# Kernel optimization log

Measured on AMD Instinct MI355X. Metric: run time of the kernel, lower is better.

Reference implementation:

```python
import jax, jax.numpy as jnp
import numpy as np

B, SQ, SE, SI, SEI = 16, 512, 512, 256, 768
D, H = 1024, 16
DK = D // H
L1, L2 = 0.5, 0.5
NEG = -1e30  # stand-in for -inf masked_fill


def setup_inputs() -> dict:
    key = jax.random.key(0)
    ks = jax.random.split(key, 32)
    f = lambda i, shp: jax.random.normal(ks[i], shp, dtype=jnp.float32)
    w = lambda i: f(i, (D, D)) * (1.0 / np.sqrt(D))
    b = lambda i: jnp.zeros((D,), jnp.float32)
    inp = {
        'q': f(0, (B, SQ, D)),
        'k_e': f(1, (B, SE, D)), 'v_e': f(2, (B, SE, D)),
        'k_i': f(3, (B, SI, D)), 'v_i': f(4, (B, SI, D)),
        'k_ei': f(5, (B, SEI, D)), 'v_ei': f(6, (B, SEI, D)),
        'mask_e': jax.random.randint(ks[7], (B, SQ, SE), 0, 2) == 1,
        'mask_ei': jax.random.randint(ks[8], (B, SQ, SEI), 0, 2) == 1,
        'e_padding_mask': jax.random.randint(ks[9], (B, SE), 0, 2) == 1,
        'ei_padding_mask': jax.random.randint(ks[10], (B, SEI), 0, 2) == 1,
        'Wq': w(11), 'bq': b(11),
        'Wke': w(12), 'bke': b(12), 'Wve': w(13), 'bve': b(13),
        'Wki': w(14), 'bki': b(14), 'Wvi': w(15), 'bvi': b(15),
        'Wkei': w(16), 'bkei': b(16), 'Wvei': w(17), 'bvei': b(17),
        'Wout': w(18), 'bout': b(18),
    }
    return inp


def _proj(x, W, b):
    # (B, S, D) -> (B, H, S, DK)
    B_, S_, _ = x.shape
    return (x @ W + b).reshape(B_, S_, H, DK).transpose(0, 2, 1, 3)


def _attn(qh, kh, vh, mask, pad_mask):
    # qh: (B,H,Sq,DK), kh/vh: (B,H,Sk,DK)
    s = jnp.einsum('bhqd,bhkd->bhqk', qh, kh) / np.sqrt(DK)
    if mask is not None:
        s = jnp.where(mask[:, None, :, :], NEG, s)
    if pad_mask is not None:
        s = jnp.where(pad_mask[:, None, None, :], NEG, s)
    w = jax.nn.softmax(s, axis=-1)
    # dropout in original is applied to a discarded temp (eval / no-op)
    return jnp.einsum('bhqk,bhkd->bhqd', w, vh), w


def reference(q, k_e, k_i, k_ei, v_e, v_i, v_ei,
              mask_e, mask_ei, e_padding_mask, ei_padding_mask,
              Wq, bq, Wke, bke, Wve, bve, Wki, bki, Wvi, bvi,
              Wkei, bkei, Wvei, bvei, Wout, bout):
    qh = _proj(q, Wq, bq)
    o_e, aw_e = _attn(qh, _proj(k_e, Wke, bke), _proj(v_e, Wve, bve), mask_e, e_padding_mask)
    o_i, aw_i = _attn(qh, _proj(k_i, Wki, bki), _proj(v_i, Wvi, bvi), None, None)
    o_ei, _ = _attn(qh, _proj(k_ei, Wkei, bkei), _proj(v_ei, Wvei, bvei), mask_ei, ei_padding_mask)
    scores = o_e + L1 * o_i + L2 * o_ei  # (B,H,Sq,DK)
    concat = scores.transpose(0, 2, 1, 3).reshape(B, SQ, D)
    output = concat @ Wout + bout
    return output, aw_e, aw_i
```

## Files before the change

### kernel.cpp

```cpp
#include <hip/hip_runtime.h>
#include <stdint.h>

typedef __attribute__((ext_vector_type(8))) short bf16x8;
typedef __attribute__((ext_vector_type(4))) short s16x4;
typedef __attribute__((ext_vector_type(4))) float f32x4;

__device__ __forceinline__ short f2bf(float f){
  unsigned x = __float_as_uint(f);
  unsigned r = (x + 0x7fffu + ((x >> 16) & 1u)) >> 16;
  return (short)r;
}

__device__ __forceinline__ void g2l16(const void* g, void* l){
  __builtin_amdgcn_global_load_lds(
      (const __attribute__((address_space(1))) unsigned int*)(unsigned long long)(uintptr_t)g,
      (__attribute__((address_space(3))) unsigned int*)(unsigned int)(uintptr_t)l,
      16, 0, 0);
}

struct C4 { const float* in[4]; short* out[4]; int n8[4]; };
__global__ __launch_bounds__(256) void cvt4(C4 c){
  const int z = blockIdx.z;
  const int i = blockIdx.x * 256 + threadIdx.x;
  if (i >= c.n8[z]) return;
  const float4* p = (const float4*)c.in[z] + (size_t)i * 2;
  const float4 a = p[0], b = p[1];
  bf16x8 v;
  v[0] = f2bf(a.x); v[1] = f2bf(a.y); v[2] = f2bf(a.z); v[3] = f2bf(a.w);
  v[4] = f2bf(b.x); v[5] = f2bf(b.y); v[6] = f2bf(b.z); v[7] = f2bf(b.w);
  *(bf16x8*)(c.out[z] + (size_t)i * 8) = v;
}

__global__ __launch_bounds__(256)
void make_bits(const int* __restrict__ mask, const int* __restrict__ pad,
               unsigned* __restrict__ bits, int SK){
  const int s = blockIdx.x * 256 + threadIdx.x;
  const size_t row = blockIdx.y;
  const int b = (int)(row >> 9);
  const bool v = (mask[row * SK + s] != 0) || (pad[(size_t)b * SK + s] != 0);
  unsigned long long bal = __ballot(v);
  const int lane = threadIdx.x & 63;
  if ((lane & 31) == 0)
    bits[(row * SK + s) >> 5] = (unsigned)(bal >> (lane & 32));
}

struct W8 { const float* w[8]; };
__global__ __launch_bounds__(256) void pack_w8(W8 ws8, short* __restrict__ out){
  const int m = blockIdx.y;
  const float* __restrict__ W = ws8.w[m];
  short* o = out + (size_t)m * 1048576 + (size_t)blockIdx.x * 4096;
  const int kt = blockIdx.x & 31, nt = blockIdx.x >> 5;
  const int t = threadIdx.x;
  #pragma unroll
  for (int i = 0; i < 16; ++i){
    int flat = i * 256 + t;
    int kl = flat >> 7;
    int nl = flat & 127;
    o[nl * 32 + kl] = f2bf(W[(size_t)(kt * 32 + kl) * 1024 + nt * 128 + nl]);
  }
}

struct GSeg { const short* A; const short* Wp; const float* bias; void* C; int om; int S; int mt; };
struct G4 { GSeg s[4]; };
__global__ __launch_bounds__(256)
void gemm128b(G4 g){
  const GSeg sg = g.s[blockIdx.z];
  if (blockIdx.x >= sg.mt) return;
  __shared__ short sA[2][4096];
  __shared__ short sB[2][4096];
  const int t = threadIdx.x;
  const int m0 = blockIdx.x * 128;
  const int nt = blockIdx.y;
  const int n0 = nt * 128;
  const int w = t >> 6, lane = t & 63, lr = lane & 15, lg = lane >> 4;
  const int wm = (w >> 1) * 64, wn = (w & 1) * 64;

  const int arow  = t >> 2;
  const int acol8 = (t & 3) * 8;
  const short* Ag = sg.A + (size_t)(m0 + arow) * 1024 + acol8;
  const short* Bg = sg.Wp + (size_t)nt * 32 * 4096 + t * 8;

  f32x4 acc[4][4] = {};

  {
    g2l16(Ag, sA[0] + t * 8);
    g2l16(Ag + 64 * 1024, sA[0] + 2048 + t * 8);
    g2l16(Bg, sB[0] + t * 8);
    g2l16(Bg + 2048, sB[0] + 2048 + t * 8);
  }

  int cur = 0;
  for (int kt = 0; kt < 32; ++kt){
    __syncthreads();
    if (kt < 31){
      const int kn = kt + 1;
      g2l16(Ag + kn * 32, sA[cur ^ 1] + t * 8);
      g2l16(Ag + 64 * 1024 + kn * 32, sA[cur ^ 1] + 2048 + t * 8);
      const short* bt = Bg + (size_t)kn * 4096;
      g2l16(bt, sB[cur ^ 1] + t * 8);
      g2l16(bt + 2048, sB[cur ^ 1] + 2048 + t * 8);
    }

    bf16x8 af[4], bfr[4];
    #pragma unroll
    for (int mi = 0; mi < 4; ++mi)
      af[mi] = *(const bf16x8*)&sA[cur][(wm + mi * 16 + lr) * 32 + lg * 8];
    #pragma unroll
    for (int ni = 0; ni < 4; ++ni)
      bfr[ni] = *(const bf16x8*)&sB[cur][(wn + ni * 16 + lr) * 32 + lg * 8];
    #pragma unroll
    for (int mi = 0; mi < 4; ++mi)
      #pragma unroll
      for (int ni = 0; ni < 4; ++ni)
        acc[mi][ni] = __builtin_amdgcn_mfma_f32_16x16x32_bf16(
            af[mi], bfr[ni], acc[mi][ni], 0, 0, 0);
    cur ^= 1;
  }

  #pragma unroll
  for (int ni = 0; ni < 4; ++ni){
    const int n = n0 + wn + ni * 16 + lr;
    const float bv = sg.bias[n];
    #pragma unroll
    for (int mi = 0; mi < 4; ++mi){
      const int mb = m0 + wm + mi * 16 + lg * 4;
      if (sg.om == 0){
        short* C = (short*)sg.C;
        #pragma unroll
        for (int j = 0; j < 4; ++j)
          C[(size_t)(mb + j) * 1024 + n] = f2bf(acc[mi][ni][j] + bv);
      } else if (sg.om == 1){
        short* C = (short*)sg.C;
        const int bb = mb / sg.S, sb = mb % sg.S;
        const int hh = n >> 6, dk = n & 63;
        s16x4 pk;
        #pragma unroll
        for (int j = 0; j < 4; ++j) pk[j] = f2bf(acc[mi][ni][j] + bv);
        *(s16x4*)&C[(((size_t)bb * 16 + hh) * 64 + dk) * sg.S + sb] = pk;
      } else {
        float* C = (float*)sg.C;
        #pragma unroll
        for (int j = 0; j < 4; ++j)
          C[(size_t)(mb + j) * 1024 + n] = acc[mi][ni][j] + bv;
      }
    }
  }
}

template<int SK, bool HAS_BIAS, bool SINGLE>
__device__ __forceinline__ void attn_mod(
    const short* __restrict__ Kp, const short* __restrict__ Vt,
    const unsigned* __restrict__ bits, float* __restrict__ aw,
    const bf16x8 (&qf)[2], f32x4 (&tot)[4], float wgt,
    short* sK, short* sV, short* sPw,
    int b, int h, int qw, int w, int lane, int lr, int lg){
  constexpr int NT  = SK / 128;
  constexpr int SKW = SK / 32;
  static_assert((NT & 1) == 0, "buffer-parity argument needs even NT");

  const int kchunk = (lane & 7) ^ ((lane >> 3) & 7);
  const short* Ksrc = Kp + ((size_t)b * SK + w * 16 + (lane >> 3)) * 1024 + h * 64 + kchunk * 8;
  const short* Vsrc = Vt + ((size_t)(b * 16 + h)) * 64 * SK;
  const int ldoff = w * 1024 + lane * 8;

  const unsigned* bitrow[4];
  if (HAS_BIAS){
    #pragma unroll
    for (int j = 0; j < 4; ++j)
      bitrow[j] = bits + ((size_t)(b * 512 + qw + lg * 4 + j)) * SKW;
  }

  float lrow[4];
  #pragma unroll
  for (int j = 0; j < 4; ++j) lrow[j] = 0.f;
  f32x4 acco[4] = {};

#define SKB(c) (sK + (c) * 8192)
#define SVB(c) (sV + (c) * 8192)
#define STAGE_K(c, s0) do{ \
    g2l16(Ksrc + (size_t)(s0) * 1024, SKB(c) + ldoff); \
    g2l16(Ksrc + (size_t)((s0) + 8) * 1024, SKB(c) + ldoff + 512); }while(0)
#define STAGE_V(c, s0) do{ \
    const int dd0 = w * 8 + (lane >> 4); \
    const int cg0 = (lane & 15) ^ (dd0 & 15); \
    g2l16(Vsrc + (size_t)dd0 * SK + (s0) + cg0 * 8, SVB(c) + ldoff); \
    const int dd1 = dd0 + 4; \
    const int cg1 = (lane & 15) ^ (dd1 & 15); \
    g2l16(Vsrc + (size_t)dd1 * SK + (s0) + cg1 * 8, SVB(c) + ldoff + 512); }while(0)

  if (!SINGLE){
    STAGE_K(0, 0);
    int cur = 0;
    for (int tt = 0; tt < NT; ++tt){
      __syncthreads();
      if (tt + 1 < NT) STAGE_K(cur ^ 1, (tt + 1) * 128);
      const short* kb = SKB(cur);

      f32x4 accs[8];
      #pragma unroll
      for (int si = 0; si < 8; ++si){
        f32x4 a = {};
        #pragma unroll
        for (int dt = 0; dt < 2; ++dt){
          bf16x8 kf = *(const bf16x8*)&kb[(si * 16 + lr) * 64 + ((dt * 4 + lg) ^ (lr & 7)) * 8];
          a = __builtin_amdgcn_mfma_f32_16x16x32_bf16(qf[dt], kf, a, 0, 0, 0);
        }
        accs[si] = a;
      }

      #pragma unroll
      for (int j = 0; j < 4; ++j){
        unsigned wb[4];
        if (HAS_BIAS){
          #pragma unroll
          for (int sp = 0; sp < 4; ++sp) wb[sp] = bitrow[j][tt * 4 + sp];
        }
        float ssum = 0.f;
        #pragma unroll
        for (int si = 0; si < 8; ++si){
          float v = accs[si][j] * 0.125f;
          if (HAS_BIAS && ((wb[si >> 1] >> ((si & 1) * 16 + lr)) & 1u)) v = -1e30f;
          ssum += __expf(v);
        }
        lrow[j] += ssum;
      }
      cur ^= 1;
    }

    #pragma unroll
    for (int j = 0; j < 4; ++j){
      #pragma unroll
      for (int d = 1; d < 16; d <<= 1) lrow[j] += __shfl_xor(lrow[j], d);
    }
    float rinv[4];
    #pragma unroll
    for (int j = 0; j < 4; ++j) rinv[j] = lrow[j] > 0.f ? 1.0f / lrow[j] : 0.f;

    STAGE_K(0, 0);
    STAGE_V(0, 0);
    cur = 0;
    for (int tt = 0; tt < NT; ++tt){
      const int s0 = tt * 128;
      __syncthreads();
      if (tt + 1 < NT){ STAGE_K(cur ^ 1, s0 + 128); STAGE_V(cur ^ 1, s0 + 128); }
      const short* kb = SKB(cur);
      const short* vb = SVB(cur);

      f32x4 accs[8];
      #pragma unroll
      for (int si = 0; si < 8; ++si){
        f32x4 a = {};
        #pragma unroll
        for (int dt = 0; dt < 2; ++dt){
          bf16x8 kf = *(const bf16x8*)&kb[(si * 16 + lr) * 64 + ((dt * 4 + lg) ^ (lr & 7)) * 8];
          a = __builtin_amdgcn_mfma_f32_16x16x32_bf16(qf[dt], kf, a, 0, 0, 0);
        }
        accs[si] = a;
      }

      #pragma unroll
      for (int half = 0; half < 2; ++half){
        #pragma unroll
        for (int j = 0; j < 4; ++j){
          unsigned wb[2];
          if (HAS_BIAS){
            #pragma unroll
            for (int sp = 0; sp < 2; ++sp) wb[sp] = bitrow[j][tt * 4 + half * 2 + sp];
          }
          const int qq = lg * 4 + j;
          float* awrow = aw + (((size_t)(b * 16 + h)) * 512 + qw + qq) * SK + s0 + half * 64 + lr;
          #pragma unroll
          for (int si2 = 0; si2 < 4; ++si2){
            const int si = half * 4 + si2;
            float v = accs[si][j] * 0.125f;
            if (HAS_BIAS && ((wb[si2 >> 1] >> ((si2 & 1) * 16 + lr)) & 1u)) v = -1e30f;
            const float p = __expf(v) * rinv[j];
            __builtin_nontemporal_store(p, &awrow[si2 * 16]);
            sPw[qq * 64 + (((si2 * 2 + (lr >> 3)) ^ (qq & 7)) * 8) + (lr & 7)] = f2bf(p);
          }
        }
        #pragma unroll
        for (int kt2 = 0; kt2 < 2; ++kt2){
          const int kt = half * 2 + kt2;
          bf16x8 pa = *(const bf16x8*)&sPw[lr * 64 + (((kt2 * 4 + lg) ^ (lr & 7)) * 8)];
          #pragma unroll
          for (int ni = 0; ni < 4; ++ni){
            bf16x8 vf = *(const bf16x8*)&vb[(ni * 16 + lr) * 128 + ((kt * 4 + lg) ^ lr) * 8];
            acco[ni] = __builtin_amdgcn_mfma_f32_16x16x32_bf16(pa, vf, acco[ni], 0, 0, 0);
          }
        }
      }
      cur ^= 1;
    }

    #pragma unroll
    for (int ni = 0; ni < 4; ++ni)
      #pragma unroll
      for (int j = 0; j < 4; ++j)
        tot[ni][j] += wgt * acco[ni][j];
  } else {
    STAGE_K(0, 0);
    STAGE_V(0, 0);
    int cur = 0;
    for (int tt = 0; tt < NT; ++tt){
      const int s0 = tt * 128;
      __syncthreads();
      if (tt + 1 < NT){ STAGE_K(cur ^ 1, s0 + 128); STAGE_V(cur ^ 1, s0 + 128); }
      const short* kb = SKB(cur);
      const short* vb = SVB(cur);

      f32x4 accs[8];
      #pragma unroll
      for (int si = 0; si < 8; ++si){
        f32x4 a = {};
        #pragma unroll
        for (int dt = 0; dt < 2; ++dt){
          bf16x8 kf = *(const bf16x8*)&kb[(si * 16 + lr) * 64 + ((dt * 4 + lg) ^ (lr & 7)) * 8];
          a = __builtin_amdgcn_mfma_f32_16x16x32_bf16(qf[dt], kf, a, 0, 0, 0);
        }
        accs[si] = a;
      }

      #pragma unroll
      for (int half = 0; half < 2; ++half){
        #pragma unroll
        for (int j = 0; j < 4; ++j){
          unsigned wb[2];
          if (HAS_BIAS){
            #pragma unroll
            for (int sp = 0; sp < 2; ++sp) wb[sp] = bitrow[j][tt * 4 + half * 2 + sp];
          }
          const int qq = lg * 4 + j;
          float ls = 0.f;
          #pragma unroll
          for (int si2 = 0; si2 < 4; ++si2){
            const int si = half * 4 + si2;
            float v = accs[si][j] * 0.125f;
            if (HAS_BIAS && ((wb[si2 >> 1] >> ((si2 & 1) * 16 + lr)) & 1u)) v = -1e30f;
            const float p = __expf(v);
            ls += p;
            sPw[qq * 64 + (((si2 * 2 + (lr >> 3)) ^ (qq & 7)) * 8) + (lr & 7)] = f2bf(p);
          }
          lrow[j] += ls;
        }
        #pragma unroll
        for (int kt2 = 0; kt2 < 2; ++kt2){
          const int kt = half * 2 + kt2;
          bf16x8 pa = *(const bf16x8*)&sPw[lr * 64 + (((kt2 * 4 + lg) ^ (lr & 7)) * 8)];
          #pragma unroll
          for (int ni = 0; ni < 4; ++ni){
            bf16x8 vf = *(const bf16x8*)&vb[(ni * 16 + lr) * 128 + ((kt * 4 + lg) ^ lr) * 8];
            acco[ni] = __builtin_amdgcn_mfma_f32_16x16x32_bf16(pa, vf, acco[ni], 0, 0, 0);
          }
        }
      }
      cur ^= 1;
    }

    #pragma unroll
    for (int j = 0; j < 4; ++j){
      #pragma unroll
      for (int d = 1; d < 16; d <<= 1) lrow[j] += __shfl_xor(lrow[j], d);
      const float r = lrow[j] > 0.f ? wgt / lrow[j] : 0.f;
      #pragma unroll
      for (int ni = 0; ni < 4; ++ni) tot[ni][j] += r * acco[ni][j];
    }
  }
#undef SKB
#undef SVB
#undef STAGE_K
#undef STAGE_V
}

__global__ __launch_bounds__(512)
void attn_fused(const short* __restrict__ Qp,
                const short* __restrict__ Kep, const short* __restrict__ Vte,
                const unsigned* __restrict__ bits_e, float* __restrict__ aw_e,
                const short* __restrict__ Kip, const short* __restrict__ Vti,
                float* __restrict__ aw_i,
                const short* __restrict__ Keip, const short* __restrict__ Vtei,
                const unsigned* __restrict__ bits_ei,
                short* __restrict__ concat){
  __shared__ short sK[2 * 8192];
  __shared__ short sV[2 * 8192];
  __shared__ short sP[8192];

  const int bid = blockIdx.x;
  const int qt = bid >> 8;
  const int g  = bid & 255;
  const int h = g & 15, b = g >> 4;
  const int q0 = qt * 128;
  const int t = threadIdx.x, w = t >> 6, lane = t & 63;
  const int lr = lane & 15, lg = lane >> 4;
  const int qw = q0 + w * 16;
  short* sPw = sP + w * 1024;

  const short* Qb = Qp + ((size_t)(b * 512 + qw + lr)) * 1024 + h * 64;
  bf16x8 qf[2];
  qf[0] = *(const bf16x8*)&Qb[lg * 8];
  qf[1] = *(const bf16x8*)&Qb[32 + lg * 8];

  f32x4 tot[4] = {};

  attn_mod<512, true , false>(Kep,  Vte,  bits_e,  aw_e, qf, tot, 1.0f,
                              sK, sV, sPw, b, h, qw, w, lane, lr, lg);
  attn_mod<256, false, false>(Kip,  Vti,  nullptr, aw_i, qf, tot, 0.5f,
                              sK, sV, sPw, b, h, qw, w, lane, lr, lg);
  attn_mod<768, true , true >(Keip, Vtei, bits_ei, nullptr, qf, tot, 0.5f,
                              sK, sV, sPw, b, h, qw, w, lane, lr, lg);

  #pragma unroll
  for (int ni = 0; ni < 4; ++ni)
    #pragma unroll
    for (int j = 0; j < 4; ++j){
      const size_t addr = ((size_t)(b * 512 + qw + lg * 4 + j)) * 1024 + h * 64 + ni * 16 + lr;
      concat[addr] = f2bf(tot[ni][j]);
    }
}

extern "C" void kernel_launch(void* const* d_in, const int* in_sizes, int n_in,
                              void* d_out, int out_size, void* d_ws, size_t ws_size,
                              hipStream_t stream){
  const float* q    = (const float*)d_in[0];
  const float* k_e  = (const float*)d_in[1];
  const float* v_e  = (const float*)d_in[2];
  const float* k_i  = (const float*)d_in[3];
  const float* v_i  = (const float*)d_in[4];
  const float* k_ei = (const float*)d_in[5];
  const float* v_ei = (const float*)d_in[6];
  const int* mask_e  = (const int*)d_in[7];
  const int* mask_ei = (const int*)d_in[8];
  const int* pad_e   = (const int*)d_in[9];
  const int* pad_ei  = (const int*)d_in[10];
  const float* Wq   = (const float*)d_in[11]; const float* bq   = (const float*)d_in[12];
  const float* Wke  = (const float*)d_in[13]; const float* bke  = (const float*)d_in[14];
  const float* Wve  = (const float*)d_in[15]; const float* bve  = (const float*)d_in[16];
  const float* Wki  = (const float*)d_in[17]; const float* bki  = (const float*)d_in[18];
  const float* Wvi  = (const float*)d_in[19]; const float* bvi  = (const float*)d_in[20];
  const float* Wkei = (const float*)d_in[21]; const float* bkei = (const float*)d_in[22];
  const float* Wvei = (const float*)d_in[23]; const float* bvei = (const float*)d_in[24];
  const float* Wout = (const float*)d_in[25]; const float* bout = (const float*)d_in[26];

  char* ws = (char*)d_ws;
  const size_t MB = 1048576;
  short* PW     = (short*)(ws);
  short* StA0   = (short*)(ws + 16 * MB);
  short* StA1   = (short*)(ws + 32 * MB);
  short* StA2   = (short*)(ws + 48 * MB);
  short* StB0   = (short*)(ws + 16 * MB);
  short* StB1   = (short*)(ws + 24 * MB);
  short* StC0   = (short*)(ws + 32 * MB);
  short* StC1   = (short*)(ws + 56 * MB);
  unsigned* bits_e  = (unsigned*)(ws + 80 * MB);
  unsigned* bits_ei = (unsigned*)(ws + 82 * MB);
  short* Qp     = (short*)(ws + 85 * MB);
  short* Kep    = (short*)(ws + 101 * MB);
  short* Kip    = (short*)(ws + 117 * MB);
  short* Keip   = (short*)(ws + 125 * MB);
  short* Vte    = (short*)(ws + 149 * MB);
  short* Vti    = (short*)(ws + 165 * MB);
  short* Vtei   = (short*)(ws + 173 * MB);
  short* concat = (short*)(ws + 16 * MB);

  float* out0 = (float*)d_out;
  float* aw_e = out0 + 8388608;
  float* aw_i = out0 + 75497472;

  W8 w8;
  w8.w[0] = Wq;  w8.w[1] = Wke;  w8.w[2] = Wve;  w8.w[3] = Wki;
  w8.w[4] = Wvi; w8.w[5] = Wkei; w8.w[6] = Wvei; w8.w[7] = Wout;
  pack_w8<<<dim3(256, 8), 256, 0, stream>>>(w8, PW);

  {
    C4 c;
    c.in[0] = q;   c.out[0] = StA0; c.n8[0] = 1048576;
    c.in[1] = k_e; c.out[1] = StA1; c.n8[1] = 1048576;
    c.in[2] = v_e; c.out[2] = StA2; c.n8[2] = 1048576;
    c.in[3] = q;   c.out[3] = StA0; c.n8[3] = 0;
    cvt4<<<dim3(4096, 1, 3), 256, 0, stream>>>(c);
    G4 gg;
    gg.s[0] = {StA0, PW + 0 * 1048576, bq,  Qp,  0, 512, 64};
    gg.s[1] = {StA1, PW + 1 * 1048576, bke, Kep, 0, 512, 64};
    gg.s[2] = {StA2, PW + 2 * 1048576, bve, Vte, 1, 512, 64};
    gg.s[3] = gg.s[0];
    gemm128b<<<dim3(64, 8, 3), 256, 0, stream>>>(gg);
  }
  {
    C4 c;
    c.in[0] = k_i;  c.out[0] = StB0; c.n8[0] = 524288;
    c.in[1] = v_i;  c.out[1] = StB1; c.n8[1] = 524288;
    c.in[2] = k_ei; c.out[2] = StC0; c.n8[2] = 1572864;
    c.in[3] = v_ei; c.out[3] = StC1; c.n8[3] = 1572864;
    cvt4<<<dim3(6144, 1, 4), 256, 0, stream>>>(c);
    G4 gg;
    gg.s[0] = {StB0, PW + 3 * 1048576, bki,  Kip,  0, 256, 32};
    gg.s[1] = {StB1, PW + 4 * 1048576, bvi,  Vti,  1, 256, 32};
    gg.s[2] = {StC0, PW + 5 * 1048576, bkei, Keip, 0, 768, 96};
    gg.s[3] = {StC1, PW + 6 * 1048576, bvei, Vtei, 1, 768, 96};
    gemm128b<<<dim3(96, 8, 4), 256, 0, stream>>>(gg);
  }

  make_bits<<<dim3(2, 8192), 256, 0, stream>>>(mask_e,  pad_e,  bits_e,  512);
  make_bits<<<dim3(3, 8192), 256, 0, stream>>>(mask_ei, pad_ei, bits_ei, 768);

  attn_fused<<<1024, 512, 0, stream>>>(Qp, Kep, Vte, bits_e, aw_e,
                                       Kip, Vti, aw_i, Keip, Vtei, bits_ei, concat);

  {
    G4 gg;
    gg.s[0] = {concat, PW + 7 * 1048576, bout, out0, 2, 512, 64};
    gg.s[1] = gg.s[0]; gg.s[2] = gg.s[0]; gg.s[3] = gg.s[0];
    gemm128b<<<dim3(64, 8, 1), 256, 0, stream>>>(gg);
  }
}
```

Baseline: 524.1 us.

## Merge conversion, GEMM and mask-bit kernels into one multi-role launcher with overlapping stages

Replaces the separate cvt4, gemm128b and make_bits kernels with a single mixk kernel whose z-dimension selects a role (GEMM, fp32-to-bf16 conversion, or mask bit packing). Conversions for the second group of inputs now run in the same launch as the first group's projections, and the mask bit packing runs alongside the last projections, so independent work overlaps and there are fewer launches. The 1/sqrt(dk) scale is folded into the packed Wq and its bias, which removes a multiply per score in attention. Workspace offsets are rearranged so the concurrently live buffers do not alias, at the cost of a larger struct argument and grid-stride loops in the conversion and mask paths.

```diff
diff --git a/kernel.cpp b/kernel.cpp
--- a/kernel.cpp
+++ b/kernel.cpp
@@ -18,35 +18,10 @@
       16, 0, 0);
 }
 
-struct C4 { const float* in[4]; short* out[4]; int n8[4]; };
-__global__ __launch_bounds__(256) void cvt4(C4 c){
-  const int z = blockIdx.z;
-  const int i = blockIdx.x * 256 + threadIdx.x;
-  if (i >= c.n8[z]) return;
-  const float4* p = (const float4*)c.in[z] + (size_t)i * 2;
-  const float4 a = p[0], b = p[1];
-  bf16x8 v;
-  v[0] = f2bf(a.x); v[1] = f2bf(a.y); v[2] = f2bf(a.z); v[3] = f2bf(a.w);
-  v[4] = f2bf(b.x); v[5] = f2bf(b.y); v[6] = f2bf(b.z); v[7] = f2bf(b.w);
-  *(bf16x8*)(c.out[z] + (size_t)i * 8) = v;
-}
-
-__global__ __launch_bounds__(256)
-void make_bits(const int* __restrict__ mask, const int* __restrict__ pad,
-               unsigned* __restrict__ bits, int SK){
-  const int s = blockIdx.x * 256 + threadIdx.x;
-  const size_t row = blockIdx.y;
-  const int b = (int)(row >> 9);
-  const bool v = (mask[row * SK + s] != 0) || (pad[(size_t)b * SK + s] != 0);
-  unsigned long long bal = __ballot(v);
-  const int lane = threadIdx.x & 63;
-  if ((lane & 31) == 0)
-    bits[(row * SK + s) >> 5] = (unsigned)(bal >> (lane & 32));
-}
-
 struct W8 { const float* w[8]; };
 __global__ __launch_bounds__(256) void pack_w8(W8 ws8, short* __restrict__ out){
   const int m = blockIdx.y;
+  const float scl = (m == 0) ? 0.125f : 1.0f;
   const float* __restrict__ W = ws8.w[m];
   short* o = out + (size_t)m * 1048576 + (size_t)blockIdx.x * 4096;
   const int kt = blockIdx.x & 31, nt = blockIdx.x >> 5;
@@ -56,18 +31,23 @@
     int flat = i * 256 + t;
     int kl = flat >> 7;
     int nl = flat & 127;
-    o[nl * 32 + kl] = f2bf(W[(size_t)(kt * 32 + kl) * 1024 + nt * 128 + nl]);
-  }
-}
-
-struct GSeg { const short* A; const short* Wp; const float* bias; void* C; int om; int S; int mt; };
-struct G4 { GSeg s[4]; };
-__global__ __launch_bounds__(256)
-void gemm128b(G4 g){
-  const GSeg sg = g.s[blockIdx.z];
-  if (blockIdx.x >= sg.mt) return;
-  __shared__ short sA[2][4096];
-  __shared__ short sB[2][4096];
+    o[nl * 32 + kl] = f2bf(W[(size_t)(kt * 32 + kl) * 1024 + nt * 128 + nl] * scl);
+  }
+}
+
+struct GSeg { const short* A; const short* Wp; const float* bias; void* C;
+              int om; int S; int mt; float bs; };
+struct Big {
+  GSeg g[4];
+  const float* cin[4]; short* cout[4]; int n8[4];
+  const int* me; const int* pe; unsigned* be;
+  const int* mi; const int* pi; unsigned* bi;
+  int act[8];
+};
+
+__device__ __forceinline__ void gemm_core(const GSeg sg,
+                                          short (*sA)[4096], short (*sB)[4096]){
+  if ((int)blockIdx.x >= sg.mt) return;
   const int t = threadIdx.x;
   const int m0 = blockIdx.x * 128;
   const int nt = blockIdx.y;
@@ -82,12 +62,10 @@
 
   f32x4 acc[4][4] = {};
 
-  {
-    g2l16(Ag, sA[0] + t * 8);
-    g2l16(Ag + 64 * 1024, sA[0] + 2048 + t * 8);
-    g2l16(Bg, sB[0] + t * 8);
-    g2l16(Bg + 2048, sB[0] + 2048 + t * 8);
-  }
+  g2l16(Ag, sA[0] + t * 8);
+  g2l16(Ag + 64 * 1024, sA[0] + 2048 + t * 8);
+  g2l16(Bg, sB[0] + t * 8);
+  g2l16(Bg + 2048, sB[0] + 2048 + t * 8);
 
   int cur = 0;
   for (int kt = 0; kt < 32; ++kt){
@@ -120,7 +98,7 @@
   #pragma unroll
   for (int ni = 0; ni < 4; ++ni){
     const int n = n0 + wn + ni * 16 + lr;
-    const float bv = sg.bias[n];
+    const float bv = sg.bias[n] * sg.bs;
     #pragma unroll
     for (int mi = 0; mi < 4; ++mi){
       const int mb = m0 + wm + mi * 16 + lg * 4;
@@ -145,6 +123,47 @@
       }
     }
   }
+}
+
+__device__ __forceinline__ void cvt_core(const float* __restrict__ in,
+                                         short* __restrict__ out, int n8){
+  const long long total = (long long)gridDim.x * gridDim.y * 256;
+  for (long long i = (long long)(blockIdx.y * gridDim.x + blockIdx.x) * 256 + threadIdx.x;
+       i < n8; i += total){
+    const float4* p = (const float4*)in + i * 2;
+    const float4 a = p[0], b = p[1];
+    bf16x8 v;
+    v[0] = f2bf(a.x); v[1] = f2bf(a.y); v[2] = f2bf(a.z); v[3] = f2bf(a.w);
+    v[4] = f2bf(b.x); v[5] = f2bf(b.y); v[6] = f2bf(b.z); v[7] = f2bf(b.w);
+    *(bf16x8*)(out + i * 8) = v;
+  }
+}
+
+__device__ __forceinline__ void bits_core(const int* __restrict__ mask,
+                                          const int* __restrict__ pad,
+                                          unsigned* __restrict__ bits,
+                                          int SK, int nsb, int nunits){
+  const int nb = gridDim.x * gridDim.y;
+  for (int u = blockIdx.y * gridDim.x + blockIdx.x; u < nunits; u += nb){
+    const int row = u / nsb, sb = u - row * nsb;
+    const int s = sb * 256 + threadIdx.x;
+    const int b = row >> 9;
+    const bool v = (mask[(size_t)row * SK + s] != 0) || (pad[(size_t)b * SK + s] != 0);
+    unsigned long long bal = __ballot(v);
+    const int lane = threadIdx.x & 63;
+    if ((lane & 31) == 0)
+      bits[((size_t)row * SK + s) >> 5] = (unsigned)(bal >> (lane & 32));
+  }
+}
+
+__global__ __launch_bounds__(256) void mixk(Big big){
+  __shared__ short sA[2][4096];
+  __shared__ short sB[2][4096];
+  const int a = big.act[blockIdx.z];
+  if (a < 4)       gemm_core(big.g[a], sA, sB);
+  else if (a < 8)  cvt_core(big.cin[a - 4], big.cout[a - 4], big.n8[a - 4]);
+  else if (a == 8) bits_core(big.me, big.pe, big.be, 512, 2, 16384);
+  else             bits_core(big.mi, big.pi, big.bi, 768, 3, 24576);
 }
 
 template<int SK, bool HAS_BIAS, bool SINGLE>
@@ -218,7 +237,7 @@
         float ssum = 0.f;
         #pragma unroll
         for (int si = 0; si < 8; ++si){
-          float v = accs[si][j] * 0.125f;
+          float v = accs[si][j];
           if (HAS_BIAS && ((wb[si >> 1] >> ((si & 1) * 16 + lr)) & 1u)) v = -1e30f;
           ssum += __expf(v);
         }
@@ -272,7 +291,7 @@
           #pragma unroll
           for (int si2 = 0; si2 < 4; ++si2){
             const int si = half * 4 + si2;
-            float v = accs[si][j] * 0.125f;
+            float v = accs[si][j];
             if (HAS_BIAS && ((wb[si2 >> 1] >> ((si2 & 1) * 16 + lr)) & 1u)) v = -1e30f;
             const float p = __expf(v) * rinv[j];
             __builtin_nontemporal_store(p, &awrow[si2 * 16]);
@@ -335,7 +354,7 @@
           #pragma unroll
           for (int si2 = 0; si2 < 4; ++si2){
             const int si = half * 4 + si2;
-            float v = accs[si][j] * 0.125f;
+            float v = accs[si][j];
             if (HAS_BIAS && ((wb[si2 >> 1] >> ((si2 & 1) * 16 + lr)) & 1u)) v = -1e30f;
             const float p = __expf(v);
             ls += p;
@@ -443,24 +462,24 @@
 
   char* ws = (char*)d_ws;
   const size_t MB = 1048576;
-  short* PW     = (short*)(ws);
-  short* StA0   = (short*)(ws + 16 * MB);
-  short* StA1   = (short*)(ws + 32 * MB);
-  short* StA2   = (short*)(ws + 48 * MB);
-  short* StB0   = (short*)(ws + 16 * MB);
-  short* StB1   = (short*)(ws + 24 * MB);
-  short* StC0   = (short*)(ws + 32 * MB);
-  short* StC1   = (short*)(ws + 56 * MB);
-  unsigned* bits_e  = (unsigned*)(ws + 80 * MB);
-  unsigned* bits_ei = (unsigned*)(ws + 82 * MB);
-  short* Qp     = (short*)(ws + 85 * MB);
-  short* Kep    = (short*)(ws + 101 * MB);
-  short* Kip    = (short*)(ws + 117 * MB);
-  short* Keip   = (short*)(ws + 125 * MB);
-  short* Vte    = (short*)(ws + 149 * MB);
-  short* Vti    = (short*)(ws + 165 * MB);
-  short* Vtei   = (short*)(ws + 173 * MB);
-  short* concat = (short*)(ws + 16 * MB);
+  short* PW   = (short*)(ws);
+  short* StA0 = (short*)(ws + 16 * MB);
+  short* StA1 = (short*)(ws + 32 * MB);
+  short* StA2 = (short*)(ws + 48 * MB);
+  short* Kip  = (short*)(ws + 16 * MB);
+  short* Vti  = (short*)(ws + 24 * MB);
+  short* Keip = (short*)(ws + 32 * MB);
+  unsigned* bits_e  = (unsigned*)(ws + 56 * MB);
+  unsigned* bits_ei = (unsigned*)(ws + 58 * MB);
+  short* StB0 = (short*)(ws + 64 * MB);
+  short* StB1 = (short*)(ws + 72 * MB);
+  short* StC0 = (short*)(ws + 80 * MB);
+  short* StC1 = (short*)(ws + 104 * MB);
+  short* concat = (short*)(ws + 64 * MB);
+  short* Qp   = (short*)(ws + 128 * MB);
+  short* Kep  = (short*)(ws + 144 * MB);
+  short* Vte  = (short*)(ws + 160 * MB);
+  short* Vtei = (short*)(ws + 176 * MB);
 
   float* out0 = (float*)d_out;
   float* aw_e = out0 + 8388608;
@@ -471,45 +490,49 @@
   w8.w[4] = Wvi; w8.w[5] = Wkei; w8.w[6] = Wvei; w8.w[7] = Wout;
   pack_w8<<<dim3(256, 8), 256, 0, stream>>>(w8, PW);
 
+  Big bg{};
+  bg.me = mask_e;  bg.pe = pad_e;  bg.be = bits_e;
+  bg.mi = mask_ei; bg.pi = pad_ei; bg.bi = bits_ei;
+
   {
-    C4 c;
-    c.in[0] = q;   c.out[0] = StA0; c.n8[0] = 1048576;
-    c.in[1] = k_e; c.out[1] = StA1; c.n8[1] = 1048576;
-    c.in[2] = v_e; c.out[2] = StA2; c.n8[2] = 1048576;
-    c.in[3] = q;   c.out[3] = StA0; c.n8[3] = 0;
-    cvt4<<<dim3(4096, 1, 3), 256, 0, stream>>>(c);
-    G4 gg;
-    gg.s[0] = {StA0, PW + 0 * 1048576, bq,  Qp,  0, 512, 64};
-    gg.s[1] = {StA1, PW + 1 * 1048576, bke, Kep, 0, 512, 64};
-    gg.s[2] = {StA2, PW + 2 * 1048576, bve, Vte, 1, 512, 64};
-    gg.s[3] = gg.s[0];
-    gemm128b<<<dim3(64, 8, 3), 256, 0, stream>>>(gg);
+    Big c = bg;
+    c.cin[0] = q;   c.cout[0] = StA0; c.n8[0] = 1048576;
+    c.cin[1] = k_e; c.cout[1] = StA1; c.n8[1] = 1048576;
+    c.cin[2] = v_e; c.cout[2] = StA2; c.n8[2] = 1048576;
+    c.act[0] = 4; c.act[1] = 5; c.act[2] = 6;
+    mixk<<<dim3(96, 8, 3), 256, 0, stream>>>(c);
   }
   {
-    C4 c;
-    c.in[0] = k_i;  c.out[0] = StB0; c.n8[0] = 524288;
-    c.in[1] = v_i;  c.out[1] = StB1; c.n8[1] = 524288;
-    c.in[2] = k_ei; c.out[2] = StC0; c.n8[2] = 1572864;
-    c.in[3] = v_ei; c.out[3] = StC1; c.n8[3] = 1572864;
-    cvt4<<<dim3(6144, 1, 4), 256, 0, stream>>>(c);
-    G4 gg;
-    gg.s[0] = {StB0, PW + 3 * 1048576, bki,  Kip,  0, 256, 32};
-    gg.s[1] = {StB1, PW + 4 * 1048576, bvi,  Vti,  1, 256, 32};
-    gg.s[2] = {StC0, PW + 5 * 1048576, bkei, Keip, 0, 768, 96};
-    gg.s[3] = {StC1, PW + 6 * 1048576, bvei, Vtei, 1, 768, 96};
-    gemm128b<<<dim3(96, 8, 4), 256, 0, stream>>>(gg);
-  }
-
-  make_bits<<<dim3(2, 8192), 256, 0, stream>>>(mask_e,  pad_e,  bits_e,  512);
-  make_bits<<<dim3(3, 8192), 256, 0, stream>>>(mask_ei, pad_ei, bits_ei, 768);
+    Big c = bg;
+    c.g[0] = {StA0, PW + 0 * 1048576, bq,  Qp,  0, 512, 64, 0.125f};
+    c.g[1] = {StA1, PW + 1 * 1048576, bke, Kep, 0, 512, 64, 1.0f};
+    c.g[2] = {StA2, PW + 2 * 1048576, bve, Vte, 1, 512, 64, 1.0f};
+    c.cin[0] = k_i;  c.cout[0] = StB0; c.n8[0] = 524288;
+    c.cin[1] = v_i;  c.cout[1] = StB1; c.n8[1] = 524288;
+    c.cin[2] = k_ei; c.cout[2] = StC0; c.n8[2] = 1572864;
+    c.cin[3] = v_ei; c.cout[3] = StC1; c.n8[3] = 1572864;
+    c.act[0] = 0; c.act[1] = 1; c.act[2] = 2;
+    c.act[3] = 4; c.act[4] = 5; c.act[5] = 6; c.act[6] = 7;
+    mixk<<<dim3(96, 8, 7), 256, 0, stream>>>(c);
+  }
+  {
+    Big c = bg;
+    c.g[0] = {StB0, PW + 3 * 1048576, bki,  Kip,  0, 256, 32, 1.0f};
+    c.g[1] = {StB1, PW + 4 * 1048576, bvi,  Vti,  1, 256, 32, 1.0f};
+    c.g[2] = {StC0, PW + 5 * 1048576, bkei, Keip, 0, 768, 96, 1.0f};
+    c.g[3] = {StC1, PW + 6 * 1048576, bvei, Vtei, 1, 768, 96, 1.0f};
+    c.act[0] = 0; c.act[1] = 1; c.act[2] = 2; c.act[3] = 3;
+    c.act[4] = 8; c.act[5] = 9;
+    mixk<<<dim3(96, 8, 6), 256, 0, stream>>>(c);
+  }
 
   attn_fused<<<1024, 512, 0, stream>>>(Qp, Kep, Vte, bits_e, aw_e,
                                        Kip, Vti, aw_i, Keip, Vtei, bits_ei, concat);
 
   {
-    G4 gg;
-    gg.s[0] = {concat, PW + 7 * 1048576, bout, out0, 2, 512, 64};
-    gg.s[1] = gg.s[0]; gg.s[2] = gg.s[0]; gg.s[3] = gg.s[0];
-    gemm128b<<<dim3(64, 8, 1), 256, 0, stream>>>(gg);
-  }
-}
+    Big c = bg;
+    c.g[0] = {concat, PW + 7 * 1048576, bout, out0, 2, 512, 64, 1.0f};
+    c.act[0] = 0;
+    mixk<<<dim3(64, 8, 1), 256, 0, stream>>>(c);
+  }
+}
```

Result: no change. 523.6 us, median of 2 (-0.1%).
